# Kernel tuning notes

Measured on AMD Instinct MI355X. Metric: run time of the kernel, lower is better.

## Reference

```python
import jax, jax.numpy as jnp
import numpy as np

V, E, H, W, S, T, B = 10000, 256, 512, 256, 512, 128, 64


def setup_inputs() -> dict:
    key = jax.random.key(0)
    ks = jax.random.split(key, 17)
    def rn(k, shape, s=0.08):
        return jax.random.normal(k, shape, jnp.float32) * s
    return {
        "tokens": jax.random.randint(ks[0], (B, S), 0, V),
        "dec_h0": jax.random.normal(ks[1], (B, H), jnp.float32),
        "emb_table": rn(ks[2], (V, E), 1.0),
        "enc_Wih": rn(ks[3], (4 * H, E)),
        "enc_Whh": rn(ks[4], (4 * H, H)),
        "enc_bih": rn(ks[5], (4 * H,)),
        "enc_bhh": rn(ks[6], (4 * H,)),
        "dec_Wih": rn(ks[7], (4 * H, E)),
        "dec_Whh": rn(ks[8], (4 * H, H)),
        "dec_bih": rn(ks[9], (4 * H,)),
        "dec_bhh": rn(ks[10], (4 * H,)),
        "W1_w": rn(ks[11], (W, H)),
        "W1_b": rn(ks[12], (W,)),
        "W2_w": rn(ks[13], (W, H)),
        "W2_b": rn(ks[14], (W,)),
        "vt_w": rn(ks[15], (1, W)),
        "vt_b": rn(ks[16], (1,)),
    }


def _lstm_cell(x, h, c, Wih, Whh, bih, bhh):
    # PyTorch gate order: input, forget, cell(g), output
    gates = x @ Wih.T + h @ Whh.T + bih + bhh
    i, f, g, o = jnp.split(gates, 4, axis=-1)
    c = jax.nn.sigmoid(f) * c + jax.nn.sigmoid(i) * jnp.tanh(g)
    h = jax.nn.sigmoid(o) * jnp.tanh(c)
    return h, c


def reference(tokens, dec_h0, emb_table, enc_Wih, enc_Whh, enc_bih, enc_bhh,
              dec_Wih, dec_Whh, dec_bih, dec_bhh, W1_w, W1_b, W2_w, W2_b,
              vt_w, vt_b):
    emb = emb_table[tokens]                       # [B,S,E]
    x_sbe = jnp.swapaxes(emb, 0, 1)               # [S,B,E] time-major
    bsz = tokens.shape[0]
    h0 = jnp.zeros((bsz, enc_Whh.shape[1]), emb.dtype)

    def enc_step(carry, x):
        h, c = carry
        h, c = _lstm_cell(x, h, c, enc_Wih, enc_Whh, enc_bih, enc_bhh)
        return (h, c), h

    _, enc_states = jax.lax.scan(enc_step, (h0, h0), x_sbe)   # [S,B,H]

    # W1(encoder_states) is constant across decoder steps -> hoist it
    blend1 = enc_states @ W1_w.T + W1_b            # [S,B,W]
    c0 = enc_states[-1]                            # original uses last enc state as cell init
    dec_in = jnp.zeros((bsz, emb_table.shape[1]), emb.dtype)  # never updated in original

    def dec_step(carry, _):
        h, c = carry
        h, c = _lstm_cell(dec_in, h, c, dec_Wih, dec_Whh, dec_bih, dec_bhh)
        blend2 = h @ W2_w.T + W2_b                 # [B,W]
        u = (jnp.tanh(blend1 + blend2[None]) @ vt_w.T)[..., 0] + vt_b[0]  # [S,B]
        logp = jax.nn.log_softmax(u.T, axis=1)     # [B,S], softmax over seq positions
        return (h, c), logp

    _, probs = jax.lax.scan(dec_step, (dec_h0, c0), None, length=T)  # [T,B,S]
    return jnp.swapaxes(probs, 0, 1)               # [B,T,S]
```

## Files before the change

### kernel.cpp

```cpp
#include <hip/hip_runtime.h>
#include <hip/hip_bf16.h>
#include <cstdint>
#include <cstddef>

typedef __bf16 bf16_t;
typedef __bf16 bf16x8 __attribute__((ext_vector_type(8)));
typedef float  f32x4  __attribute__((ext_vector_type(4)));

#define NB 64
#define NS 512
#define NTD 128
#define NE 256
#define NH 512
#define NG 2048
#define NW 256

#define HSTEP_DW 16384u

__device__ __forceinline__ float sigm_f(float x) { return 1.f / (1.f + __expf(-x)); }
__device__ __forceinline__ float tanh_f(float x) {
  float e = __expf(2.f * x);
  return 1.f - 2.f / (e + 1.f);
}
__device__ __forceinline__ float bits2f(uint32_t b16) {
  uint32_t u = b16 << 16;
  return __builtin_bit_cast(float, u);
}
__device__ __forceinline__ uint32_t packh(float a, float b) {
  uint16_t lo = __builtin_bit_cast(uint16_t, (bf16_t)a);
  uint16_t hi = __builtin_bit_cast(uint16_t, (bf16_t)b);
  return (uint32_t)lo | ((uint32_t)hi << 16);
}

__global__ __launch_bounds__(256) void pack_b(const float* __restrict__ src,
                                              bf16_t* __restrict__ dst,
                                              int N, int K) {
  int idx = blockIdx.x * 256 + threadIdx.x;
  if (idx >= N * K) return;
  int n = idx / K, k = idx - n * K;
  int lane = (((k & 31) >> 3) << 4) | (n & 15);
  size_t o = ((((size_t)(n >> 4) * (K >> 5)) + (k >> 5)) * 64 + lane) * 8 + (k & 7);
  dst[o] = (bf16_t)src[idx];
}

__global__ __launch_bounds__(256) void gather_emb(const int* __restrict__ tokens,
                                                  const float* __restrict__ table,
                                                  bf16_t* __restrict__ embfrag) {
  int idx = blockIdx.x * 256 + threadIdx.x;
  int row = idx >> 5, e0 = (idx & 31) << 3;
  int b = row & 63, s = row >> 6;
  int tok = tokens[b * NS + s];
  const float4* p = (const float4*)(table + (size_t)tok * NE + e0);
  float4 v0 = p[0], v1 = p[1];
  bf16x8 v;
  v[0] = (bf16_t)v0.x; v[1] = (bf16_t)v0.y; v[2] = (bf16_t)v0.z; v[3] = (bf16_t)v0.w;
  v[4] = (bf16_t)v1.x; v[5] = (bf16_t)v1.y; v[6] = (bf16_t)v1.z; v[7] = (bf16_t)v1.w;
  int mt = row >> 4;
  int ks = e0 >> 5;
  int lane = (b & 15) | (((e0 >> 3) & 3) << 4);
  *(bf16x8*)(embfrag + ((size_t)(mt * 8 + ks) * 64 + lane) * 8) = v;
}

__global__ __launch_bounds__(256) void pack_h0(const float* __restrict__ src,
                                               uint32_t* __restrict__ dst) {
  int idx = blockIdx.x * 256 + threadIdx.x;
  int b = idx >> 8, jp = idx & 255;
  int j = jp * 2;
  float lo = src[(size_t)b * NH + j], hi = src[(size_t)b * NH + j + 1];
  int bg = b >> 4, bl = b & 15, ks = j >> 5;
  int lane = bl | (((j >> 3) & 3) << 4);
  dst[((size_t)bg * 16 + ks) * 256 + lane * 4 + ((j >> 1) & 3)] = packh(lo, hi);
}

template <typename OutT, int KS, int MT>
__global__ __launch_bounds__(256) void gemm_fa2(const bf16_t* __restrict__ A,
                                                const bf16_t* __restrict__ Bp,
                                                OutT* __restrict__ out,
                                                const float* __restrict__ bias1,
                                                const float* __restrict__ bias2,
                                                int N) {
  int lane = threadIdx.x & 63, w = threadIdx.x >> 6;
  int nt = blockIdx.x * 4 + w;
  int mt0 = blockIdx.y * MT;
  bf16x8 bfr[KS];
  const bf16_t* bp = Bp + ((size_t)nt * KS * 64 + lane) * 8;
#pragma unroll
  for (int ks = 0; ks < KS; ++ks) bfr[ks] = *(const bf16x8*)(bp + (size_t)ks * 512);
  int col = (nt << 4) + (lane & 15);
  float bs = bias1[col] + (bias2 ? bias2[col] : 0.f);
  for (int m = 0; m < MT; ++m) {
    int mt = mt0 + m;
    const bf16_t* ap = A + (size_t)mt * (KS * 512) + lane * 8;
    f32x4 acc = {0.f, 0.f, 0.f, 0.f};
#pragma unroll
    for (int ks = 0; ks < KS; ++ks)
      acc = __builtin_amdgcn_mfma_f32_16x16x32_bf16(
          *(const bf16x8*)(ap + (size_t)ks * 512), bfr[ks], acc, 0, 0, 0);
    int rbase = (mt << 4) + ((lane >> 4) << 2);
#pragma unroll
    for (int r = 0; r < 4; ++r)
      out[(size_t)(rbase + r) * N + col] = (OutT)(acc[r] + bs);
  }
}

template <bool USE_XIH>
__global__ __launch_bounds__(256) void lstm_chain(
    const bf16_t* __restrict__ Wp,
    const bf16_t* __restrict__ xih,
    const float* __restrict__ bih, const float* __restrict__ bhh,
    uint32_t* __restrict__ hfrag,
    const uint32_t* __restrict__ c0frag,
    uint32_t* __restrict__ flags,
    int T) {
  __shared__ bf16_t wlds[8 * 8192];
  __shared__ float gl[4][16][36];
  int tid = threadIdx.x, lane = tid & 63, wv = tid >> 6;
  int bg = blockIdx.x >> 4, slice = blockIdx.x & 15;

  for (int l = 0; l < 8; ++l) {
    int g = l >> 1, p = l & 1;
    const bf16_t* src = Wp + (size_t)(g * 32 + slice * 2 + p) * 8192;
    bf16_t* dst = wlds + (size_t)l * 8192;
    for (int i = tid; i < 1024; i += 256)
      *(bf16x8*)(dst + (size_t)i * 8) = *(const bf16x8*)(src + (size_t)i * 8);
  }

  int ub = tid >> 4, uj2 = tid & 15;
  int j_lo = slice * 32 + uj2 * 2;
  int lane_f = ub | ((uj2 >> 2) << 4);
  float c0 = 0.f, c1 = 0.f;
  if (c0frag != nullptr) {
    uint32_t d = c0frag[((size_t)bg * 16 + slice) * 256 + lane_f * 4 + (uj2 & 3)];
    c0 = bits2f(d & 0xffffu);
    c1 = bits2f(d >> 16);
  }
  float bsum[4][2];
  if (!USE_XIH) {
#pragma unroll
    for (int g = 0; g < 4; ++g) {
      bsum[g][0] = bih[g * NH + j_lo] + bhh[g * NH + j_lo];
      bsum[g][1] = bih[g * NH + j_lo + 1] + bhh[g * NH + j_lo + 1];
    }
  }
  __syncthreads();

  const uint64_t* hq = (const uint64_t*)hfrag;
  uint32_t* fl = flags + bg * 16;

  for (int t = 0; t < T; ++t) {
    uint32_t xd[4];
    if (USE_XIH) {
      const uint32_t* xr = (const uint32_t*)xih +
          ((size_t)(t * 64 + bg * 16 + ub)) * 1024 + slice * 16 + uj2;
#pragma unroll
      for (int g = 0; g < 4; ++g) xd[g] = xr[(size_t)g * 256];
    }
    if (t > 0) {
      uint32_t tgt = (uint32_t)t;
      bool ok;
      do {
        uint32_t f = tgt;
        if (lane < 16 && lane != (uint32_t)slice)
          f = __hip_atomic_load(fl + lane, __ATOMIC_RELAXED,
                                __HIP_MEMORY_SCOPE_AGENT);
        ok = __all(f >= tgt);
      } while (!ok);
    }
    const uint64_t* hb = hq + ((size_t)t * 4 + bg) * 2048 + lane * 2;
    uint64_t aq[16][2];
#pragma unroll
    for (int ks = 0; ks < 16; ++ks) {
      aq[ks][0] = __hip_atomic_load(hb + (size_t)ks * 128,
                                    __ATOMIC_RELAXED, __HIP_MEMORY_SCOPE_AGENT);
      aq[ks][1] = __hip_atomic_load(hb + (size_t)ks * 128 + 1,
                                    __ATOMIC_RELAXED, __HIP_MEMORY_SCOPE_AGENT);
    }
    const bf16_t* wl = wlds + (size_t)(wv * 2) * 8192 + lane * 8;
    f32x4 acc0 = {0.f, 0.f, 0.f, 0.f}, acc1 = {0.f, 0.f, 0.f, 0.f};
#pragma unroll
    for (int ks = 0; ks < 16; ++ks) {
      union { uint64_t q[2]; bf16x8 v; } u;
      u.q[0] = aq[ks][0]; u.q[1] = aq[ks][1];
      acc0 = __builtin_amdgcn_mfma_f32_16x16x32_bf16(
          u.v, *(const bf16x8*)(wl + (size_t)ks * 512), acc0, 0, 0, 0);
      acc1 = __builtin_amdgcn_mfma_f32_16x16x32_bf16(
          u.v, *(const bf16x8*)(wl + 8192 + (size_t)ks * 512), acc1, 0, 0, 0);
    }
    int cc = lane & 15, rb = (lane >> 4) << 2;
#pragma unroll
    for (int r = 0; r < 4; ++r) {
      gl[wv][rb + r][cc] = acc0[r];
      gl[wv][rb + r][16 + cc] = acc1[r];
    }
    __syncthreads();

    float p[4][2];
#pragma unroll
    for (int g = 0; g < 4; ++g) {
      p[g][0] = gl[g][ub][uj2 * 2];
      p[g][1] = gl[g][ub][uj2 * 2 + 1];
    }
    if (USE_XIH) {
#pragma unroll
      for (int g = 0; g < 4; ++g) {
        p[g][0] += bits2f(xd[g] & 0xffffu);
        p[g][1] += bits2f(xd[g] >> 16);
      }
    } else {
#pragma unroll
      for (int g = 0; g < 4; ++g) { p[g][0] += bsum[g][0]; p[g][1] += bsum[g][1]; }
    }
    float i0 = sigm_f(p[0][0]), f0 = sigm_f(p[1][0]);
    float g0 = tanh_f(p[2][0]), o0 = sigm_f(p[3][0]);
    c0 = f0 * c0 + i0 * g0;
    float h0 = o0 * tanh_f(c0);
    float i1 = sigm_f(p[0][1]), f1 = sigm_f(p[1][1]);
    float g1 = tanh_f(p[2][1]), o1 = sigm_f(p[3][1]);
    c1 = f1 * c1 + i1 * g1;
    float h1 = o1 * tanh_f(c1);
    __hip_atomic_store(hfrag + ((size_t)(t + 1) * 4 + bg) * 4096 +
                           slice * 256 + lane_f * 4 + (uj2 & 3),
                       packh(h0, h1), __ATOMIC_RELAXED, __HIP_MEMORY_SCOPE_AGENT);
    __syncthreads();
    if (tid == 0)
      __hip_atomic_store(fl + slice, (uint32_t)(t + 1),
                         __ATOMIC_RELAXED, __HIP_MEMORY_SCOPE_AGENT);
  }
}

__global__ __launch_bounds__(256) void attn_kernel(const bf16_t* __restrict__ blend1,
                                                   const float* __restrict__ blend2,
                                                   const float* __restrict__ vt_w,
                                                   float* __restrict__ out) {
  __shared__ float s_vt[272], s_b2[272], s_u[512], s_red[8];
  int t = blockIdx.x >> 6;
  int b = blockIdx.x & 63;
  int tid = threadIdx.x, lane = tid & 63, wv = tid >> 6;
  {
    int ww = tid;
    int pi = ww + ((ww >> 6) << 2);
    s_vt[pi] = vt_w[ww];
    s_b2[pi] = blend2[(size_t)(t * 64 + b) * NW + ww];
  }
  __syncthreads();
  int wgrp = lane >> 4, sgrp = lane & 15;
  int base = wgrp * 68;
  for (int it = 0; it < 8; ++it) {
    int s = it * 64 + wv * 16 + sgrp;
    const bf16_t* row = blend1 + ((size_t)s * NB + b) * NW + wgrp * 64;
    float val = 0.f;
#pragma unroll
    for (int c8 = 0; c8 < 8; ++c8) {
      bf16x8 v = *(const bf16x8*)(row + c8 * 8);
#pragma unroll
      for (int jx = 0; jx < 8; ++jx) {
        int wi = base + c8 * 8 + jx;
        val += s_vt[wi] * tanh_f((float)v[jx] + s_b2[wi]);
      }
    }
    val += __shfl_xor(val, 16, 64);
    val += __shfl_xor(val, 32, 64);
    if (wgrp == 0) s_u[it * 64 + wv * 16 + sgrp] = val;
  }
  __syncthreads();
  float a = s_u[tid], bb2 = s_u[tid + 256];
  float m = fmaxf(a, bb2);
#pragma unroll
  for (int off = 1; off < 64; off <<= 1) m = fmaxf(m, __shfl_xor(m, off, 64));
  if (lane == 0) s_red[wv] = m;
  __syncthreads();
  m = fmaxf(fmaxf(s_red[0], s_red[1]), fmaxf(s_red[2], s_red[3]));
  float e = __expf(a - m) + __expf(bb2 - m);
#pragma unroll
  for (int off = 1; off < 64; off <<= 1) e += __shfl_xor(e, off, 64);
  if (lane == 0) s_red[4 + wv] = e;
  __syncthreads();
  float lz = m + logf(s_red[4] + s_red[5] + s_red[6] + s_red[7]);
  size_t ob = ((size_t)b * NTD + t) * NS;
  out[ob + tid] = a - lz;
  out[ob + tid + 256] = bb2 - lz;
}

extern "C" void kernel_launch(void* const* d_in, const int* in_sizes, int n_in,
                              void* d_out, int out_size, void* d_ws, size_t ws_size,
                              hipStream_t stream) {
  const int*   tokens    = (const int*)d_in[0];
  const float* dec_h0    = (const float*)d_in[1];
  const float* emb_table = (const float*)d_in[2];
  const float* enc_Wih   = (const float*)d_in[3];
  const float* enc_Whh   = (const float*)d_in[4];
  const float* enc_bih   = (const float*)d_in[5];
  const float* enc_bhh   = (const float*)d_in[6];
  const float* dec_Whh   = (const float*)d_in[8];
  const float* dec_bih   = (const float*)d_in[9];
  const float* dec_bhh   = (const float*)d_in[10];
  const float* W1_w      = (const float*)d_in[11];
  const float* W1_b      = (const float*)d_in[12];
  const float* W2_w      = (const float*)d_in[13];
  const float* W2_b      = (const float*)d_in[14];
  const float* vt_w      = (const float*)d_in[15];
  float* out = (float*)d_out;

  char* w = (char*)d_ws;
  size_t off = 0;
  auto alloc = [&](size_t bytes) {
    size_t o = off;
    off += (bytes + 255) & ~(size_t)255;
    return o;
  };
  bf16_t* embfrag = (bf16_t*)(w + alloc((size_t)NS * NB * NE * 2));
  bf16_t* xih     = (bf16_t*)(w + alloc((size_t)NS * NB * NG * 2));
  uint32_t* enc_hf = (uint32_t*)(w + alloc((size_t)(NS + 1) * HSTEP_DW * 4));
  uint32_t* dec_hf = (uint32_t*)(w + alloc((size_t)(NTD + 1) * HSTEP_DW * 4));
  bf16_t* blend1  = (bf16_t*)(w + alloc((size_t)NS * NB * NW * 2));
  float*  blend2  = (float*)(w + alloc((size_t)NTD * NB * NW * 4));
  bf16_t* pWih    = (bf16_t*)(w + alloc((size_t)NG * NE * 2));
  bf16_t* pWhhE   = (bf16_t*)(w + alloc((size_t)NG * NH * 2));
  bf16_t* pWhhD   = (bf16_t*)(w + alloc((size_t)NG * NH * 2));
  bf16_t* pW1     = (bf16_t*)(w + alloc((size_t)NW * NH * 2));
  bf16_t* pW2     = (bf16_t*)(w + alloc((size_t)NW * NH * 2));
  uint32_t* flags = (uint32_t*)(w + alloc(512));
  (void)ws_size; (void)in_sizes; (void)n_in; (void)out_size;

  hipMemsetAsync(flags, 0, 512, stream);
  hipMemsetAsync(enc_hf, 0, HSTEP_DW * 4, stream);

  pack_b<<<(NG * NE) / 256, 256, 0, stream>>>(enc_Wih, pWih, NG, NE);
  pack_b<<<(NG * NH) / 256, 256, 0, stream>>>(enc_Whh, pWhhE, NG, NH);
  pack_b<<<(NG * NH) / 256, 256, 0, stream>>>(dec_Whh, pWhhD, NG, NH);
  pack_b<<<(NW * NH) / 256, 256, 0, stream>>>(W1_w, pW1, NW, NH);
  pack_b<<<(NW * NH) / 256, 256, 0, stream>>>(W2_w, pW2, NW, NH);

  gather_emb<<<(NS * NB * (NE / 8)) / 256, 256, 0, stream>>>(tokens, emb_table, embfrag);
  pack_h0<<<64, 256, 0, stream>>>(dec_h0, dec_hf);

  gemm_fa2<bf16_t, 8, 16><<<dim3(128 / 4, 2048 / 16), 256, 0, stream>>>(
      embfrag, pWih, xih, enc_bih, enc_bhh, NG);

  lstm_chain<true><<<64, 256, 0, stream>>>(pWhhE, xih, nullptr, nullptr,
                                           enc_hf, nullptr, flags, NS);

  gemm_fa2<bf16_t, 16, 16><<<dim3(16 / 4, 2048 / 16), 256, 0, stream>>>(
      (const bf16_t*)(enc_hf + HSTEP_DW), pW1, blend1, W1_b, nullptr, NW);

  lstm_chain<false><<<64, 256, 0, stream>>>(pWhhD, nullptr, dec_bih, dec_bhh,
                                            dec_hf, enc_hf + (size_t)NS * HSTEP_DW,
                                            flags + 64, NTD);

  gemm_fa2<float, 16, 16><<<dim3(16 / 4, 512 / 16), 256, 0, stream>>>(
      (const bf16_t*)(dec_hf + HSTEP_DW), pW2, blend2, W2_b, nullptr, NW);

  attn_kernel<<<NTD * NB, 256, 0, stream>>>(blend1, blend2, vt_w, out);
}
```

Before: 2.866 ms.

## Fuse W1/W2 projections into LSTM chains and overlap attention with decoder

```diff
diff --git a/kernel.cpp b/kernel.cpp
--- a/kernel.cpp
+++ b/kernel.cpp
@@ -30,6 +30,22 @@
   uint16_t lo = __builtin_bit_cast(uint16_t, (bf16_t)a);
   uint16_t hi = __builtin_bit_cast(uint16_t, (bf16_t)b);
   return (uint32_t)lo | ((uint32_t)hi << 16);
+}
+__device__ __forceinline__ uint32_t aload(const uint32_t* p) {
+  return __hip_atomic_load(p, __ATOMIC_RELAXED, __HIP_MEMORY_SCOPE_AGENT);
+}
+__device__ __forceinline__ uint64_t aload64(const uint64_t* p) {
+  return __hip_atomic_load(p, __ATOMIC_RELAXED, __HIP_MEMORY_SCOPE_AGENT);
+}
+__device__ __forceinline__ void astore(uint32_t* p, uint32_t v) {
+  __hip_atomic_store(p, v, __ATOMIC_RELAXED, __HIP_MEMORY_SCOPE_AGENT);
+}
+__device__ __forceinline__ void astoref(float* p, float v) {
+  __hip_atomic_store((uint32_t*)p, __builtin_bit_cast(uint32_t, v),
+                     __ATOMIC_RELAXED, __HIP_MEMORY_SCOPE_AGENT);
+}
+__device__ __forceinline__ float aloadf(const float* p) {
+  return __builtin_bit_cast(float, aload((const uint32_t*)p));
 }
 
 __global__ __launch_bounds__(256) void pack_b(const float* __restrict__ src,
@@ -103,17 +119,15 @@
   }
 }
 
-template <bool USE_XIH>
-__global__ __launch_bounds__(256) void lstm_chain(
-    const bf16_t* __restrict__ Wp,
-    const bf16_t* __restrict__ xih,
-    const float* __restrict__ bih, const float* __restrict__ bhh,
-    uint32_t* __restrict__ hfrag,
-    const uint32_t* __restrict__ c0frag,
-    uint32_t* __restrict__ flags,
-    int T) {
+__global__ __launch_bounds__(256) void enc_chain(
+    const bf16_t* __restrict__ Wp, const bf16_t* __restrict__ xih,
+    const bf16_t* __restrict__ W1p, const float* __restrict__ W1_b,
+    uint32_t* __restrict__ hfrag, uint32_t* __restrict__ flags,
+    bf16_t* __restrict__ blend1) {
   __shared__ bf16_t wlds[8 * 8192];
+  __shared__ bf16_t w1lds[8192];
   __shared__ float gl[4][16][36];
+  const int T = NS;
   int tid = threadIdx.x, lane = tid & 63, wv = tid >> 6;
   int bg = blockIdx.x >> 4, slice = blockIdx.x & 15;
 
@@ -124,161 +138,294 @@
     for (int i = tid; i < 1024; i += 256)
       *(bf16x8*)(dst + (size_t)i * 8) = *(const bf16x8*)(src + (size_t)i * 8);
   }
+  {
+    const bf16_t* src = W1p + (size_t)slice * 8192;
+    for (int i = tid; i < 1024; i += 256)
+      *(bf16x8*)(w1lds + (size_t)i * 8) = *(const bf16x8*)(src + (size_t)i * 8);
+  }
 
   int ub = tid >> 4, uj2 = tid & 15;
-  int j_lo = slice * 32 + uj2 * 2;
   int lane_f = ub | ((uj2 >> 2) << 4);
   float c0 = 0.f, c1 = 0.f;
-  if (c0frag != nullptr) {
+  float b1bias = W1_b[slice * 16 + (lane & 15)];
+  __syncthreads();
+
+  const uint64_t* hq = (const uint64_t*)hfrag;
+  uint32_t* fl = flags + bg * 16;
+
+  for (int t = 0; t <= T; ++t) {
+    uint32_t xd[4];
+    if (t < T) {
+      const uint32_t* xr = (const uint32_t*)xih +
+          ((size_t)(t * 64 + bg * 16 + ub)) * 1024 + slice * 16 + uj2;
+#pragma unroll
+      for (int g = 0; g < 4; ++g) xd[g] = xr[(size_t)g * 256];
+    }
+    if (t > 0) {
+      if (wv == 0) {
+        uint32_t tgt = (uint32_t)t;
+        bool ok;
+        do {
+          uint32_t f = tgt;
+          if (lane < 16 && lane != (uint32_t)slice) f = aload(fl + lane);
+          ok = __all(f >= tgt);
+        } while (!ok);
+      }
+      __syncthreads();
+    }
+    const uint64_t* hb = hq + ((size_t)t * 4 + bg) * 2048 + lane * 2;
+    uint64_t aq[16][2];
+#pragma unroll
+    for (int ks = 0; ks < 16; ++ks) {
+      aq[ks][0] = aload64(hb + (size_t)ks * 128);
+      aq[ks][1] = aload64(hb + (size_t)ks * 128 + 1);
+    }
+    if (t >= 1 && wv == 0) {
+      f32x4 bacc = {0.f, 0.f, 0.f, 0.f};
+#pragma unroll
+      for (int ks = 0; ks < 16; ++ks) {
+        union { uint64_t q[2]; bf16x8 v; } u;
+        u.q[0] = aq[ks][0]; u.q[1] = aq[ks][1];
+        bacc = __builtin_amdgcn_mfma_f32_16x16x32_bf16(
+            u.v, *(const bf16x8*)(w1lds + (size_t)ks * 512 + lane * 8), bacc, 0, 0, 0);
+      }
+      int col = slice * 16 + (lane & 15);
+      int rb = (lane >> 4) << 2;
+      size_t rowb = (size_t)(t - 1) * 64 + bg * 16 + rb;
+#pragma unroll
+      for (int r = 0; r < 4; ++r)
+        blend1[(rowb + r) * 256 + col] = (bf16_t)(bacc[r] + b1bias);
+    }
+    if (t < T) {
+      const bf16_t* wl = wlds + (size_t)(wv * 2) * 8192 + lane * 8;
+      f32x4 acc0 = {0.f, 0.f, 0.f, 0.f}, acc1 = {0.f, 0.f, 0.f, 0.f};
+#pragma unroll
+      for (int ks = 0; ks < 16; ++ks) {
+        union { uint64_t q[2]; bf16x8 v; } u;
+        u.q[0] = aq[ks][0]; u.q[1] = aq[ks][1];
+        acc0 = __builtin_amdgcn_mfma_f32_16x16x32_bf16(
+            u.v, *(const bf16x8*)(wl + (size_t)ks * 512), acc0, 0, 0, 0);
+        acc1 = __builtin_amdgcn_mfma_f32_16x16x32_bf16(
+            u.v, *(const bf16x8*)(wl + 8192 + (size_t)ks * 512), acc1, 0, 0, 0);
+      }
+      int cc = lane & 15, rb = (lane >> 4) << 2;
+#pragma unroll
+      for (int r = 0; r < 4; ++r) {
+        gl[wv][rb + r][cc] = acc0[r];
+        gl[wv][rb + r][16 + cc] = acc1[r];
+      }
+      __syncthreads();
+      float p[4][2];
+#pragma unroll
+      for (int g = 0; g < 4; ++g) {
+        p[g][0] = gl[g][ub][uj2 * 2] + bits2f(xd[g] & 0xffffu);
+        p[g][1] = gl[g][ub][uj2 * 2 + 1] + bits2f(xd[g] >> 16);
+      }
+      float i0 = sigm_f(p[0][0]), f0 = sigm_f(p[1][0]);
+      float g0 = tanh_f(p[2][0]), o0 = sigm_f(p[3][0]);
+      c0 = f0 * c0 + i0 * g0;
+      float h0 = o0 * tanh_f(c0);
+      float i1 = sigm_f(p[0][1]), f1 = sigm_f(p[1][1]);
+      float g1 = tanh_f(p[2][1]), o1 = sigm_f(p[3][1]);
+      c1 = f1 * c1 + i1 * g1;
+      float h1 = o1 * tanh_f(c1);
+      astore(hfrag + ((size_t)(t + 1) * 4 + bg) * 4096 +
+                 slice * 256 + lane_f * 4 + (uj2 & 3), packh(h0, h1));
+      __syncthreads();
+      if (tid == 0) astore(fl + slice, (uint32_t)(t + 1));
+    }
+  }
+}
+
+__global__ __launch_bounds__(256) void dec_attn(
+    const bf16_t* __restrict__ Wp, const float* __restrict__ bih,
+    const float* __restrict__ bhh, const bf16_t* __restrict__ W2p,
+    const float* __restrict__ W2_b, uint32_t* __restrict__ hfrag,
+    const uint32_t* __restrict__ c0frag, uint32_t* __restrict__ hflags,
+    uint32_t* __restrict__ bl2f, const bf16_t* __restrict__ blend1,
+    float* __restrict__ blend2, const float* __restrict__ vt_w,
+    float* __restrict__ out) {
+  union SM {
+    struct { bf16_t wlds[8 * 8192]; bf16_t w2lds[8192]; float gl[4][16][36]; } c;
+    struct { float vt[272], b2[272], u[512], red[8]; } a;
+  };
+  __shared__ SM sm;
+  const int T = NTD;
+  int tid = threadIdx.x, lane = tid & 63, wv = tid >> 6;
+
+  if (blockIdx.x < 64) {
+    int bg = blockIdx.x >> 4, slice = blockIdx.x & 15;
+    for (int l = 0; l < 8; ++l) {
+      int g = l >> 1, p = l & 1;
+      const bf16_t* src = Wp + (size_t)(g * 32 + slice * 2 + p) * 8192;
+      bf16_t* dst = sm.c.wlds + (size_t)l * 8192;
+      for (int i = tid; i < 1024; i += 256)
+        *(bf16x8*)(dst + (size_t)i * 8) = *(const bf16x8*)(src + (size_t)i * 8);
+    }
+    {
+      const bf16_t* src = W2p + (size_t)slice * 8192;
+      for (int i = tid; i < 1024; i += 256)
+        *(bf16x8*)(sm.c.w2lds + (size_t)i * 8) = *(const bf16x8*)(src + (size_t)i * 8);
+    }
+    int ub = tid >> 4, uj2 = tid & 15;
+    int j_lo = slice * 32 + uj2 * 2;
+    int lane_f = ub | ((uj2 >> 2) << 4);
     uint32_t d = c0frag[((size_t)bg * 16 + slice) * 256 + lane_f * 4 + (uj2 & 3)];
-    c0 = bits2f(d & 0xffffu);
-    c1 = bits2f(d >> 16);
-  }
-  float bsum[4][2];
-  if (!USE_XIH) {
+    float c0 = bits2f(d & 0xffffu), c1 = bits2f(d >> 16);
+    float bsum[4][2];
 #pragma unroll
     for (int g = 0; g < 4; ++g) {
       bsum[g][0] = bih[g * NH + j_lo] + bhh[g * NH + j_lo];
       bsum[g][1] = bih[g * NH + j_lo + 1] + bhh[g * NH + j_lo + 1];
     }
+    float b2bias = W2_b[slice * 16 + (lane & 15)];
+    __syncthreads();
+
+    const uint64_t* hq = (const uint64_t*)hfrag;
+    uint32_t* fl = hflags + bg * 16;
+
+    for (int t = 0; t <= T; ++t) {
+      if (t > 0) {
+        if (wv == 0) {
+          uint32_t tgt = (uint32_t)t;
+          bool ok;
+          do {
+            uint32_t f = tgt;
+            if (lane < 16 && lane != (uint32_t)slice) f = aload(fl + lane);
+            ok = __all(f >= tgt);
+          } while (!ok);
+        }
+        __syncthreads();
+      }
+      const uint64_t* hb = hq + ((size_t)t * 4 + bg) * 2048 + lane * 2;
+      uint64_t aq[16][2];
+#pragma unroll
+      for (int ks = 0; ks < 16; ++ks) {
+        aq[ks][0] = aload64(hb + (size_t)ks * 128);
+        aq[ks][1] = aload64(hb + (size_t)ks * 128 + 1);
+      }
+      if (t >= 1 && wv == 0) {
+        f32x4 bacc = {0.f, 0.f, 0.f, 0.f};
+#pragma unroll
+        for (int ks = 0; ks < 16; ++ks) {
+          union { uint64_t q[2]; bf16x8 v; } u;
+          u.q[0] = aq[ks][0]; u.q[1] = aq[ks][1];
+          bacc = __builtin_amdgcn_mfma_f32_16x16x32_bf16(
+              u.v, *(const bf16x8*)(sm.c.w2lds + (size_t)ks * 512 + lane * 8),
+              bacc, 0, 0, 0);
+        }
+        int col = slice * 16 + (lane & 15);
+        int rb = (lane >> 4) << 2;
+        size_t rowb = (size_t)(t - 1) * 64 + bg * 16 + rb;
+#pragma unroll
+        for (int r = 0; r < 4; ++r)
+          astoref(blend2 + (rowb + r) * 256 + col, bacc[r] + b2bias);
+      }
+      if (t < T) {
+        const bf16_t* wl = sm.c.wlds + (size_t)(wv * 2) * 8192 + lane * 8;
+        f32x4 acc0 = {0.f, 0.f, 0.f, 0.f}, acc1 = {0.f, 0.f, 0.f, 0.f};
+#pragma unroll
+        for (int ks = 0; ks < 16; ++ks) {
+          union { uint64_t q[2]; bf16x8 v; } u;
+          u.q[0] = aq[ks][0]; u.q[1] = aq[ks][1];
+          acc0 = __builtin_amdgcn_mfma_f32_16x16x32_bf16(
+              u.v, *(const bf16x8*)(wl + (size_t)ks * 512), acc0, 0, 0, 0);
+          acc1 = __builtin_amdgcn_mfma_f32_16x16x32_bf16(
+              u.v, *(const bf16x8*)(wl + 8192 + (size_t)ks * 512), acc1, 0, 0, 0);
+        }
+        int cc = lane & 15, rb = (lane >> 4) << 2;
+#pragma unroll
+        for (int r = 0; r < 4; ++r) {
+          sm.c.gl[wv][rb + r][cc] = acc0[r];
+          sm.c.gl[wv][rb + r][16 + cc] = acc1[r];
+        }
+        __syncthreads();
+        float p[4][2];
+#pragma unroll
+        for (int g = 0; g < 4; ++g) {
+          p[g][0] = sm.c.gl[g][ub][uj2 * 2] + bsum[g][0];
+          p[g][1] = sm.c.gl[g][ub][uj2 * 2 + 1] + bsum[g][1];
+        }
+        float i0 = sigm_f(p[0][0]), f0 = sigm_f(p[1][0]);
+        float g0 = tanh_f(p[2][0]), o0 = sigm_f(p[3][0]);
+        c0 = f0 * c0 + i0 * g0;
+        float h0 = o0 * tanh_f(c0);
+        float i1 = sigm_f(p[0][1]), f1 = sigm_f(p[1][1]);
+        float g1 = tanh_f(p[2][1]), o1 = sigm_f(p[3][1]);
+        c1 = f1 * c1 + i1 * g1;
+        float h1 = o1 * tanh_f(c1);
+        astore(hfrag + ((size_t)(t + 1) * 4 + bg) * 4096 +
+                   slice * 256 + lane_f * 4 + (uj2 & 3), packh(h0, h1));
+        __syncthreads();
+        if (tid == 0) {
+          astore(fl + slice, (uint32_t)(t + 1));
+          astore(bl2f + bg * 16 + slice, (uint32_t)t);
+        }
+      } else {
+        __syncthreads();
+        if (tid == 0) astore(bl2f + bg * 16 + slice, (uint32_t)T);
+      }
+    }
+  } else {
+    int w = blockIdx.x - 64;
+    for (int k = w; k < NTD * NB; k += 192) {
+      int t = k >> 6, b = k & 63;
+      if (wv == 0) {
+        uint32_t tgt = (uint32_t)(t + 1);
+        bool ok;
+        do {
+          uint32_t f = aload(bl2f + lane);
+          ok = __all(f >= tgt);
+          if (!ok) __builtin_amdgcn_s_sleep(16);
+        } while (!ok);
+      }
+      __syncthreads();
+      {
+        int ww = tid;
+        int pi = ww + ((ww >> 6) << 2);
+        sm.a.vt[pi] = vt_w[ww];
+        sm.a.b2[pi] = aloadf(blend2 + (size_t)(t * 64 + b) * NW + ww);
+      }
+      __syncthreads();
+      int wgrp = lane >> 4, sgrp = lane & 15;
+      int base = wgrp * 68;
+      for (int it = 0; it < 8; ++it) {
+        int s = it * 64 + wv * 16 + sgrp;
+        const bf16_t* row = blend1 + ((size_t)s * NB + b) * NW + wgrp * 64;
+        float val = 0.f;
+#pragma unroll
+        for (int c8 = 0; c8 < 8; ++c8) {
+          bf16x8 v = *(const bf16x8*)(row + c8 * 8);
+#pragma unroll
+          for (int jx = 0; jx < 8; ++jx) {
+            int wi = base + c8 * 8 + jx;
+            val += sm.a.vt[wi] * tanh_f((float)v[jx] + sm.a.b2[wi]);
+          }
+        }
+        val += __shfl_xor(val, 16, 64);
+        val += __shfl_xor(val, 32, 64);
+        if (wgrp == 0) sm.a.u[it * 64 + wv * 16 + sgrp] = val;
+      }
+      __syncthreads();
+      float a = sm.a.u[tid], bb2 = sm.a.u[tid + 256];
+      float m = fmaxf(a, bb2);
+#pragma unroll
+      for (int o = 1; o < 64; o <<= 1) m = fmaxf(m, __shfl_xor(m, o, 64));
+      if (lane == 0) sm.a.red[wv] = m;
+      __syncthreads();
+      m = fmaxf(fmaxf(sm.a.red[0], sm.a.red[1]), fmaxf(sm.a.red[2], sm.a.red[3]));
+      float e = __expf(a - m) + __expf(bb2 - m);
+#pragma unroll
+      for (int o = 1; o < 64; o <<= 1) e += __shfl_xor(e, o, 64);
+      if (lane == 0) sm.a.red[4 + wv] = e;
+      __syncthreads();
+      float lz = m + logf(sm.a.red[4] + sm.a.red[5] + sm.a.red[6] + sm.a.red[7]);
+      size_t ob = ((size_t)b * NTD + t) * NS;
+      out[ob + tid] = a - lz;
+      out[ob + tid + 256] = bb2 - lz;
+      __syncthreads();
+    }
   }
-  __syncthreads();
-
-  const uint64_t* hq = (const uint64_t*)hfrag;
-  uint32_t* fl = flags + bg * 16;
-
-  for (int t = 0; t < T; ++t) {
-    uint32_t xd[4];
-    if (USE_XIH) {
-      const uint32_t* xr = (const uint32_t*)xih +
-          ((size_t)(t * 64 + bg * 16 + ub)) * 1024 + slice * 16 + uj2;
-#pragma unroll
-      for (int g = 0; g < 4; ++g) xd[g] = xr[(size_t)g * 256];
-    }
-    if (t > 0) {
-      uint32_t tgt = (uint32_t)t;
-      bool ok;
-      do {
-        uint32_t f = tgt;
-        if (lane < 16 && lane != (uint32_t)slice)
-          f = __hip_atomic_load(fl + lane, __ATOMIC_RELAXED,
-                                __HIP_MEMORY_SCOPE_AGENT);
-        ok = __all(f >= tgt);
-      } while (!ok);
-    }
-    const uint64_t* hb = hq + ((size_t)t * 4 + bg) * 2048 + lane * 2;
-    uint64_t aq[16][2];
-#pragma unroll
-    for (int ks = 0; ks < 16; ++ks) {
-      aq[ks][0] = __hip_atomic_load(hb + (size_t)ks * 128,
-                                    __ATOMIC_RELAXED, __HIP_MEMORY_SCOPE_AGENT);
-      aq[ks][1] = __hip_atomic_load(hb + (size_t)ks * 128 + 1,
-                                    __ATOMIC_RELAXED, __HIP_MEMORY_SCOPE_AGENT);
-    }
-    const bf16_t* wl = wlds + (size_t)(wv * 2) * 8192 + lane * 8;
-    f32x4 acc0 = {0.f, 0.f, 0.f, 0.f}, acc1 = {0.f, 0.f, 0.f, 0.f};
-#pragma unroll
-    for (int ks = 0; ks < 16; ++ks) {
-      union { uint64_t q[2]; bf16x8 v; } u;
-      u.q[0] = aq[ks][0]; u.q[1] = aq[ks][1];
-      acc0 = __builtin_amdgcn_mfma_f32_16x16x32_bf16(
-          u.v, *(const bf16x8*)(wl + (size_t)ks * 512), acc0, 0, 0, 0);
-      acc1 = __builtin_amdgcn_mfma_f32_16x16x32_bf16(
-          u.v, *(const bf16x8*)(wl + 8192 + (size_t)ks * 512), acc1, 0, 0, 0);
-    }
-    int cc = lane & 15, rb = (lane >> 4) << 2;
-#pragma unroll
-    for (int r = 0; r < 4; ++r) {
-      gl[wv][rb + r][cc] = acc0[r];
-      gl[wv][rb + r][16 + cc] = acc1[r];
-    }
-    __syncthreads();
-
-    float p[4][2];
-#pragma unroll
-    for (int g = 0; g < 4; ++g) {
-      p[g][0] = gl[g][ub][uj2 * 2];
-      p[g][1] = gl[g][ub][uj2 * 2 + 1];
-    }
-    if (USE_XIH) {
-#pragma unroll
-      for (int g = 0; g < 4; ++g) {
-        p[g][0] += bits2f(xd[g] & 0xffffu);
-        p[g][1] += bits2f(xd[g] >> 16);
-      }
-    } else {
-#pragma unroll
-      for (int g = 0; g < 4; ++g) { p[g][0] += bsum[g][0]; p[g][1] += bsum[g][1]; }
-    }
-    float i0 = sigm_f(p[0][0]), f0 = sigm_f(p[1][0]);
-    float g0 = tanh_f(p[2][0]), o0 = sigm_f(p[3][0]);
-    c0 = f0 * c0 + i0 * g0;
-    float h0 = o0 * tanh_f(c0);
-    float i1 = sigm_f(p[0][1]), f1 = sigm_f(p[1][1]);
-    float g1 = tanh_f(p[2][1]), o1 = sigm_f(p[3][1]);
-    c1 = f1 * c1 + i1 * g1;
-    float h1 = o1 * tanh_f(c1);
-    __hip_atomic_store(hfrag + ((size_t)(t + 1) * 4 + bg) * 4096 +
-                           slice * 256 + lane_f * 4 + (uj2 & 3),
-                       packh(h0, h1), __ATOMIC_RELAXED, __HIP_MEMORY_SCOPE_AGENT);
-    __syncthreads();
-    if (tid == 0)
-      __hip_atomic_store(fl + slice, (uint32_t)(t + 1),
-                         __ATOMIC_RELAXED, __HIP_MEMORY_SCOPE_AGENT);
-  }
-}
-
-__global__ __launch_bounds__(256) void attn_kernel(const bf16_t* __restrict__ blend1,
-                                                   const float* __restrict__ blend2,
-                                                   const float* __restrict__ vt_w,
-                                                   float* __restrict__ out) {
-  __shared__ float s_vt[272], s_b2[272], s_u[512], s_red[8];
-  int t = blockIdx.x >> 6;
-  int b = blockIdx.x & 63;
-  int tid = threadIdx.x, lane = tid & 63, wv = tid >> 6;
-  {
-    int ww = tid;
-    int pi = ww + ((ww >> 6) << 2);
-    s_vt[pi] = vt_w[ww];
-    s_b2[pi] = blend2[(size_t)(t * 64 + b) * NW + ww];
-  }
-  __syncthreads();
-  int wgrp = lane >> 4, sgrp = lane & 15;
-  int base = wgrp * 68;
-  for (int it = 0; it < 8; ++it) {
-    int s = it * 64 + wv * 16 + sgrp;
-    const bf16_t* row = blend1 + ((size_t)s * NB + b) * NW + wgrp * 64;
-    float val = 0.f;
-#pragma unroll
-    for (int c8 = 0; c8 < 8; ++c8) {
-      bf16x8 v = *(const bf16x8*)(row + c8 * 8);
-#pragma unroll
-      for (int jx = 0; jx < 8; ++jx) {
-        int wi = base + c8 * 8 + jx;
-        val += s_vt[wi] * tanh_f((float)v[jx] + s_b2[wi]);
-      }
-    }
-    val += __shfl_xor(val, 16, 64);
-    val += __shfl_xor(val, 32, 64);
-    if (wgrp == 0) s_u[it * 64 + wv * 16 + sgrp] = val;
-  }
-  __syncthreads();
-  float a = s_u[tid], bb2 = s_u[tid + 256];
-  float m = fmaxf(a, bb2);
-#pragma unroll
-  for (int off = 1; off < 64; off <<= 1) m = fmaxf(m, __shfl_xor(m, off, 64));
-  if (lane == 0) s_red[wv] = m;
-  __syncthreads();
-  m = fmaxf(fmaxf(s_red[0], s_red[1]), fmaxf(s_red[2], s_red[3]));
-  float e = __expf(a - m) + __expf(bb2 - m);
-#pragma unroll
-  for (int off = 1; off < 64; off <<= 1) e += __shfl_xor(e, off, 64);
-  if (lane == 0) s_red[4 + wv] = e;
-  __syncthreads();
-  float lz = m + logf(s_red[4] + s_red[5] + s_red[6] + s_red[7]);
-  size_t ob = ((size_t)b * NTD + t) * NS;
-  out[ob + tid] = a - lz;
-  out[ob + tid + 256] = bb2 - lz;
 }
 
 extern "C" void kernel_launch(void* const* d_in, const int* in_sizes, int n_in,
@@ -319,10 +466,10 @@
   bf16_t* pWhhD   = (bf16_t*)(w + alloc((size_t)NG * NH * 2));
   bf16_t* pW1     = (bf16_t*)(w + alloc((size_t)NW * NH * 2));
   bf16_t* pW2     = (bf16_t*)(w + alloc((size_t)NW * NH * 2));
-  uint32_t* flags = (uint32_t*)(w + alloc(512));
+  uint32_t* flags = (uint32_t*)(w + alloc(1024));
   (void)ws_size; (void)in_sizes; (void)n_in; (void)out_size;
 
-  hipMemsetAsync(flags, 0, 512, stream);
+  hipMemsetAsync(flags, 0, 768, stream);
   hipMemsetAsync(enc_hf, 0, HSTEP_DW * 4, stream);
 
   pack_b<<<(NG * NE) / 256, 256, 0, stream>>>(enc_Wih, pWih, NG, NE);
@@ -337,18 +484,9 @@
   gemm_fa2<bf16_t, 8, 16><<<dim3(128 / 4, 2048 / 16), 256, 0, stream>>>(
       embfrag, pWih, xih, enc_bih, enc_bhh, NG);
 
-  lstm_chain<true><<<64, 256, 0, stream>>>(pWhhE, xih, nullptr, nullptr,
-                                           enc_hf, nullptr, flags, NS);
-
-  gemm_fa2<bf16_t, 16, 16><<<dim3(16 / 4, 2048 / 16), 256, 0, stream>>>(
-      (const bf16_t*)(enc_hf + HSTEP_DW), pW1, blend1, W1_b, nullptr, NW);
-
-  lstm_chain<false><<<64, 256, 0, stream>>>(pWhhD, nullptr, dec_bih, dec_bhh,
-                                            dec_hf, enc_hf + (size_t)NS * HSTEP_DW,
-                                            flags + 64, NTD);
-
-  gemm_fa2<float, 16, 16><<<dim3(16 / 4, 512 / 16), 256, 0, stream>>>(
-      (const bf16_t*)(dec_hf + HSTEP_DW), pW2, blend2, W2_b, nullptr, NW);
-
-  attn_kernel<<<NTD * NB, 256, 0, stream>>>(blend1, blend2, vt_w, out);
-}
+  enc_chain<<<64, 256, 0, stream>>>(pWhhE, xih, pW1, W1_b, enc_hf, flags, blend1);
+
+  dec_attn<<<256, 256, 0, stream>>>(pWhhD, dec_bih, dec_bhh, pW2, W2_b, dec_hf,
+                                    enc_hf + (size_t)NS * HSTEP_DW, flags + 64,
+                                    flags + 128, blend1, blend2, vt_w, out);
+}
```

Result: slower. 3.243 ms (+13.2%).
